# Kernel tuning notes

Hardware: AMD Instinct MI355X
Metric: run time of the kernel (lower is better)

## Reference

```python
import jax, jax.numpy as jnp
import numpy as np

N_NODES = 100000
N_EDGES = 640000
N_REL = 3
D_IN = 128
D_OUT = 128


def setup_inputs() -> dict:
    key = jax.random.key(0)
    ks = jax.random.split(key, 10)
    x = jax.random.normal(ks[0], (N_NODES, D_IN), dtype=jnp.float32)
    src = jax.random.randint(ks[1], (N_REL, N_EDGES), 0, N_NODES, dtype=jnp.int32)
    dst = jax.random.randint(ks[2], (N_REL, N_EDGES), 0, N_NODES, dtype=jnp.int32)
    s = 1.0 / np.sqrt(D_IN)
    W = jax.random.uniform(ks[3], (N_REL, D_IN, D_OUT), minval=-s, maxval=s, dtype=jnp.float32)
    b = jnp.zeros((N_REL, D_OUT), dtype=jnp.float32)
    sa = 1.0 / np.sqrt(D_OUT)
    Wa1 = jax.random.uniform(ks[4], (D_OUT, D_OUT), minval=-sa, maxval=sa, dtype=jnp.float32)
    ba1 = jax.random.uniform(ks[5], (D_OUT,), minval=-sa, maxval=sa, dtype=jnp.float32)
    wa2 = jax.random.uniform(ks[6], (D_OUT,), minval=-sa, maxval=sa, dtype=jnp.float32)
    return {"x": x, "src": src, "dst": dst, "W": W, "b": b,
            "Wa1": Wa1, "ba1": ba1, "wa2": wa2}


def _graph_conv(x, s, d, W_r, b_r, n):
    # DGL GraphConv, norm='both': D_out^{-1/2} -> W -> sum-aggregate -> D_in^{-1/2} -> +b
    ones = jnp.ones_like(s, dtype=x.dtype)
    deg_out = jnp.clip(jax.ops.segment_sum(ones, s, num_segments=n), 1.0)
    deg_in = jnp.clip(jax.ops.segment_sum(ones, d, num_segments=n), 1.0)
    h = (x * jax.lax.rsqrt(deg_out)[:, None]) @ W_r          # [N, D_out]
    agg = jax.ops.segment_sum(h[s], d, num_segments=n)        # gather + scatter-add
    return agg * jax.lax.rsqrt(deg_in)[:, None] + b_r


def reference(x, src, dst, W, b, Wa1, ba1, wa2):
    n = x.shape[0]
    # per-relation graph conv (loop over small fixed relation set)
    rel = jnp.stack([_graph_conv(x, src[r], dst[r], W[r], b[r], n)
                     for r in range(src.shape[0])])            # [R, N, D]
    # attention pooling over relation axis (softmax over dim 0)
    score = jnp.tanh(rel @ Wa1 + ba1) @ wa2                    # [R, N]
    attn = jax.nn.softmax(score, axis=0)[..., None]            # [R, N, 1]
    return (attn * rel).sum(axis=0)                            # [N, D]
```

## Files before the change

kernel.cpp:

```cpp
#include <hip/hip_runtime.h>

#define NN 100000
#define NE 640000
#define NR 3
#define DD 128
#define NSEG (NR * NN)
#define NBPR 782
#define NBUK (NR * NBPR)
#define BCAP 1280
#define CHUNK 8192
#define NBLK2 ((NR * NE + CHUNK - 1) / CHUNK)

typedef unsigned int u32;
typedef short bf8_t __attribute__((ext_vector_type(8)));
typedef float f4_t __attribute__((ext_vector_type(4)));

union U4 { uint4 u; bf8_t b; };

__device__ __forceinline__ u32 bfr(float f) {
  u32 u = __float_as_uint(f);
  return (u + 0x7fffu + ((u >> 16) & 1u)) >> 16;
}
__device__ __forceinline__ u32 packbf(float a, float b) {
  return bfr(a) | (bfr(b) << 16);
}
__device__ __forceinline__ float lo16(u32 u) { return __uint_as_float(u << 16); }
__device__ __forceinline__ float hi16(u32 u) { return __uint_as_float(u & 0xffff0000u); }
__device__ __forceinline__ float bf2f(u32 bits) { return __uint_as_float(bits << 16); }

__device__ __forceinline__ bf8_t ldfrag(const u32* p) {
  U4 t; t.u = *(const uint4*)p; return t.b;
}

__device__ __forceinline__ void gload_lds16(const u32* g, u32* l) {
  __builtin_amdgcn_global_load_lds((const __attribute__((address_space(1))) void*)g,
                                   (__attribute__((address_space(3))) void*)l, 16, 0, 0);
}

__global__ __launch_bounds__(256) void convert_x_kernel(const float* __restrict__ x,
                                                        u32* __restrict__ xb) {
  int i = blockIdx.x * 256 + threadIdx.x;
  if (i >= NN * 64) return;
  float2 v = ((const float2*)x)[i];
  xb[i] = packbf(v.x, v.y);
}

__global__ __launch_bounds__(512) void count_pass_kernel(const int* __restrict__ src,
                                                         const int* __restrict__ dst,
                                                         int* __restrict__ cnt_out,
                                                         int* __restrict__ cntmat) {
  __shared__ int cnt[NBUK];
  const int tid = threadIdx.x;
  for (int i = tid; i < NBUK; i += 512) cnt[i] = 0;
  __syncthreads();
  const int base = blockIdx.x * CHUNK;
  const int end = min(base + CHUNK, NR * NE);
  for (int i = base + tid; i < end; i += 512) {
    int r = i / NE;
    atomicAdd(&cnt_out[r * NN + src[i]], 1);
    atomicAdd(&cnt[r * NBPR + (dst[i] >> 7)], 1);
  }
  __syncthreads();
  for (int i = tid; i < NBUK; i += 512) cntmat[blockIdx.x * NBUK + i] = cnt[i];
}

__global__ __launch_bounds__(256) void rs_out_kernel(const int* __restrict__ cnt_out,
                                                     float* __restrict__ rs_out) {
  int i = blockIdx.x * 256 + threadIdx.x;
  if (i >= NSEG) return;
  int co = cnt_out[i]; if (co < 1) co = 1;
  rs_out[i] = rsqrtf((float)co);
}

__global__ __launch_bounds__(256) void scan_blocks_kernel(int* __restrict__ cntmat,
                                                          int* __restrict__ btot) {
  __shared__ int s[256];
  const int bk = blockIdx.x;
  const int t = threadIdx.x;
  int v = (t < NBLK2) ? cntmat[t * NBUK + bk] : 0;
  s[t] = v;
  __syncthreads();
  for (int d = 1; d < 256; d <<= 1) {
    int a = (t >= d) ? s[t - d] : 0;
    __syncthreads();
    s[t] += a;
    __syncthreads();
  }
  if (t < NBLK2) cntmat[t * NBUK + bk] = s[t] - v;
  if (t == 255) btot[bk] = s[255];
}

__global__ __launch_bounds__(256) void scan_buckets_kernel(const int* __restrict__ btot,
                                                           int* __restrict__ bucketbase) {
  __shared__ int s[256];
  const int tid = threadIdx.x;
  int v[10]; int loc = 0;
#pragma unroll
  for (int j = 0; j < 10; ++j) {
    int idx = tid * 10 + j;
    int c = (idx < NBUK) ? btot[idx] : 0;
    v[j] = c; loc += c;
  }
  s[tid] = loc;
  __syncthreads();
  for (int d = 1; d < 256; d <<= 1) {
    int t = (tid >= d) ? s[tid - d] : 0;
    __syncthreads();
    s[tid] += t;
    __syncthreads();
  }
  int run = s[tid] - loc;
#pragma unroll
  for (int j = 0; j < 10; ++j) {
    int idx = tid * 10 + j;
    if (idx < NBUK) bucketbase[idx] = run;
    run += v[j];
  }
  if (tid == 255) bucketbase[NBUK] = s[255];
}

__global__ __launch_bounds__(512) void place_pass_kernel(const int* __restrict__ src,
                                                         const int* __restrict__ dst,
                                                         const int* __restrict__ cntmat,
                                                         const int* __restrict__ bucketbase,
                                                         u32* __restrict__ bucketbuf) {
  __shared__ int cur[NBUK];
  const int tid = threadIdx.x;
  for (int i = tid; i < NBUK; i += 512)
    cur[i] = bucketbase[i] + cntmat[blockIdx.x * NBUK + i];
  __syncthreads();
  const int base = blockIdx.x * CHUNK;
  const int end = min(base + CHUNK, NR * NE);
  for (int i = base + tid; i < end; i += 512) {
    int r = i / NE;
    int d = dst[i];
    int bk = r * NBPR + (d >> 7);
    int pos = atomicAdd(&cur[bk], 1);
    bucketbuf[pos] = (u32)src[i] | ((u32)(d & 127) << 17);
  }
}

__global__ __launch_bounds__(256) void bucket_aggregate_kernel(
    const u32* __restrict__ xb, const u32* __restrict__ bucketbuf,
    const int* __restrict__ bucketbase, const float* __restrict__ rs_out,
    float* __restrict__ rs_in, u32* __restrict__ aggb) {
  __shared__ u32 eL[BCAP];
  __shared__ u32 sorted[BCAP];
  __shared__ int cntA[128], prefE[128], cur[128];
  const int tid = threadIdx.x;
  const int bk = blockIdx.x;
  const int r = bk / NBPR, bidx = bk % NBPR;
  const int node0 = bidx * 128;
  const int base = bucketbase[bk];
  const int count = min(bucketbase[bk + 1] - base, BCAP);
  if (tid < 128) cntA[tid] = 0;
  for (int i = tid; i < count; i += 256) eL[i] = bucketbuf[base + i];
  __syncthreads();
  for (int i = tid; i < count; i += 256) atomicAdd(&cntA[eL[i] >> 17], 1);
  __syncthreads();
  if (tid < 128) prefE[tid] = cntA[tid];
  __syncthreads();
  for (int d = 1; d < 128; d <<= 1) {
    int v = 0;
    if (tid < 128 && tid >= d) v = prefE[tid - d];
    __syncthreads();
    if (tid < 128) prefE[tid] += v;
    __syncthreads();
  }
  if (tid < 128) {
    int excl = prefE[tid] - cntA[tid];
    prefE[tid] = excl;
    cur[tid] = excl;
    int node = node0 + tid;
    if (node < NN) rs_in[r * NN + node] = rsqrtf((float)max(cntA[tid], 1));
  }
  __syncthreads();
  for (int i = tid; i < count; i += 256) {
    u32 v = eL[i];
    int pos = atomicAdd(&cur[v >> 17], 1);
    sorted[pos] = v & 0x1FFFFu;
  }
  __syncthreads();

  const int l16 = tid & 15, g = tid >> 4;
  const float* rsb = rs_out + r * NN;
  for (int nn = g; nn < 128; nn += 16) {
    const int node = node0 + nn;
    if (node >= NN) continue;
    const int beg = prefE[nn], cE = cntA[nn];
    float a[8] = {0.f, 0.f, 0.f, 0.f, 0.f, 0.f, 0.f, 0.f};
    int e = 0;
    for (; e + 1 < cE; e += 2) {
      int s0 = (int)sorted[beg + e], s1 = (int)sorted[beg + e + 1];
      float c0 = rsb[s0], c1 = rsb[s1];
      uint4 u0 = *(const uint4*)&xb[(size_t)s0 * 64 + l16 * 4];
      uint4 u1 = *(const uint4*)&xb[(size_t)s1 * 64 + l16 * 4];
      a[0] = fmaf(lo16(u0.x), c0, a[0]); a[1] = fmaf(hi16(u0.x), c0, a[1]);
      a[2] = fmaf(lo16(u0.y), c0, a[2]); a[3] = fmaf(hi16(u0.y), c0, a[3]);
      a[4] = fmaf(lo16(u0.z), c0, a[4]); a[5] = fmaf(hi16(u0.z), c0, a[5]);
      a[6] = fmaf(lo16(u0.w), c0, a[6]); a[7] = fmaf(hi16(u0.w), c0, a[7]);
      a[0] = fmaf(lo16(u1.x), c1, a[0]); a[1] = fmaf(hi16(u1.x), c1, a[1]);
      a[2] = fmaf(lo16(u1.y), c1, a[2]); a[3] = fmaf(hi16(u1.y), c1, a[3]);
      a[4] = fmaf(lo16(u1.z), c1, a[4]); a[5] = fmaf(hi16(u1.z), c1, a[5]);
      a[6] = fmaf(lo16(u1.w), c1, a[6]); a[7] = fmaf(hi16(u1.w), c1, a[7]);
    }
    if (e < cE) {
      int s0 = (int)sorted[beg + e];
      float c0 = rsb[s0];
      uint4 u0 = *(const uint4*)&xb[(size_t)s0 * 64 + l16 * 4];
      a[0] = fmaf(lo16(u0.x), c0, a[0]); a[1] = fmaf(hi16(u0.x), c0, a[1]);
      a[2] = fmaf(lo16(u0.y), c0, a[2]); a[3] = fmaf(hi16(u0.y), c0, a[3]);
      a[4] = fmaf(lo16(u0.z), c0, a[4]); a[5] = fmaf(hi16(u0.z), c0, a[5]);
      a[6] = fmaf(lo16(u0.w), c0, a[6]); a[7] = fmaf(hi16(u0.w), c0, a[7]);
    }
    uint4 o;
    o.x = packbf(a[0], a[1]);
    o.y = packbf(a[2], a[3]);
    o.z = packbf(a[4], a[5]);
    o.w = packbf(a[6], a[7]);
    *(uint4*)&aggb[((size_t)r * NN + node) * 64 + l16 * 4] = o;
  }
}

__global__ __launch_bounds__(256) void prep_wwa1_kernel(const float* __restrict__ W,
                                                        const float* __restrict__ Wa1,
                                                        float* __restrict__ WWa1) {
  int idx = blockIdx.x * 256 + threadIdx.x;
  if (idx >= NR * DD * DD) return;
  int r = idx >> 14, rem = idx & 16383, i = rem >> 7, c = rem & 127;
  const float* wrow = W + (r << 14) + (i << 7);
  float s = 0.f;
#pragma unroll 8
  for (int k = 0; k < DD; ++k) s = fmaf(wrow[k], Wa1[k * DD + c], s);
  WWa1[idx] = s;
}

__global__ __launch_bounds__(256) void prep_pack_kernel(const float* __restrict__ W,
                                                        const float* __restrict__ WWa1,
                                                        u32* __restrict__ wt_hi,
                                                        u32* __restrict__ wt_lo,
                                                        u32* __restrict__ wwt_hi) {
  int idx = blockIdx.x * 256 + threadIdx.x;
  if (idx >= NR * DD * 64) return;
  int r = idx >> 13, rem = idx & 8191, n = rem >> 6, ku = rem & 63;
  int k0 = ku * 2;
  int oidx = (r << 13) + ((ku >> 2) << 9) + (n << 2) + (ku & 3);
  {
    const float* M = W + (r << 14);
    float w0 = M[k0 * DD + n], w1 = M[(k0 + 1) * DD + n];
    u32 h0 = bfr(w0), h1 = bfr(w1);
    float l0 = w0 - bf2f(h0), l1 = w1 - bf2f(h1);
    wt_hi[oidx] = h0 | (h1 << 16);
    wt_lo[oidx] = packbf(l0, l1);
  }
  {
    const float* M = WWa1 + (r << 14);
    float w0 = M[k0 * DD + n], w1 = M[(k0 + 1) * DD + n];
    wwt_hi[oidx] = bfr(w0) | (bfr(w1) << 16);
  }
}

__global__ __launch_bounds__(256) void prep_bsum_kernel(const float* __restrict__ b,
                                                        const float* __restrict__ Wa1,
                                                        const float* __restrict__ ba1,
                                                        float* __restrict__ bsum) {
  int idx = blockIdx.x * 256 + threadIdx.x;
  if (idx >= NR * DD) return;
  int r = idx >> 7, c = idx & 127;
  float s = ba1[c];
#pragma unroll 8
  for (int k = 0; k < DD; ++k) s = fmaf(b[r * DD + k], Wa1[k * DD + c], s);
  bsum[idx] = s;
}

#define MFMA(a, b, c) __builtin_amdgcn_mfma_f32_16x16x32_bf16((a), (b), (c), 0, 0, 0)

__global__ __launch_bounds__(256, 2) void tail_fused_kernel(
    const u32* __restrict__ aggb, const u32* __restrict__ wt_hi,
    const u32* __restrict__ wt_lo, const u32* __restrict__ wwt_hi,
    const float* __restrict__ rs_in, const float* __restrict__ bias,
    const float* __restrict__ bsum, const float* __restrict__ wa2,
    float* __restrict__ out) {
  __shared__ u32 As[4160];
  __shared__ float scoreS[2][64];
  __shared__ float eLs[64];
  __shared__ float bL[NR][DD];
  const int tid = threadIdx.x;
  const int l = tid & 63, w = tid >> 6;
  const int wr = w >> 1, wc = w & 1;
  const int l15 = l & 15, lg = l >> 4;
  const int row0 = blockIdx.x * 64;

  for (int idx = tid; idx < NR * DD; idx += 256) bL[idx >> 7][idx & 127] = bias[idx];

  float wa2v[4];
#pragma unroll
  for (int nf = 0; nf < 4; ++nf) wa2v[nf] = wa2[wc * 64 + nf * 16 + l15];

  f4_t fo[2][4];
  float denom[2][4];
#pragma unroll
  for (int rf = 0; rf < 2; ++rf)
#pragma unroll
    for (int reg = 0; reg < 4; ++reg) {
      denom[rf][reg] = 0.f;
#pragma unroll
      for (int nf = 0; nf < 4; ++nf) fo[rf][nf][reg] = 0.f;
    }

  for (int r = 0; r < NR; ++r) {
    __syncthreads();
    const u32* Ar = aggb + (size_t)r * NN * 64;
#pragma unroll
    for (int it = 0; it < 4; ++it) {
      int s = it * 256 + tid;
      int row = s >> 4;
      int c = (s & 15) ^ (row & 7);
      int grow = min(row0 + row, NN - 1);
      gload_lds16(Ar + (size_t)grow * 64 + c * 4, &As[it * 1024 + w * 256]);
    }
    __syncthreads();

    float rsv[2][4];
#pragma unroll
    for (int rf = 0; rf < 2; ++rf)
#pragma unroll
      for (int reg = 0; reg < 4; ++reg)
        rsv[rf][reg] = rs_in[r * NN + min(row0 + wr * 32 + rf * 16 + lg * 4 + reg, NN - 1)];

    f4_t c2[2][4];
#pragma unroll
    for (int rf = 0; rf < 2; ++rf)
#pragma unroll
      for (int nf = 0; nf < 4; ++nf) c2[rf][nf] = (f4_t)0.f;
#pragma unroll
    for (int ks = 0; ks < 4; ++ks) {
      bf8_t a[2];
#pragma unroll
      for (int rf = 0; rf < 2; ++rf) {
        int m = wr * 32 + rf * 16 + l15;
        int ch = (ks * 4 + lg) ^ (m & 7);
        a[rf] = ldfrag(&As[m * 64 + ch * 4]);
      }
#pragma unroll
      for (int nf = 0; nf < 4; ++nf) {
        int n = wc * 64 + nf * 16 + l15;
        bf8_t gb = ldfrag(wwt_hi + (size_t)r * 8192 + (ks * 4 + lg) * 512 + n * 4);
#pragma unroll
        for (int rf = 0; rf < 2; ++rf) c2[rf][nf] = MFMA(a[rf], gb, c2[rf][nf]);
      }
    }

#pragma unroll
    for (int rf = 0; rf < 2; ++rf) {
      float part[4] = {0.f, 0.f, 0.f, 0.f};
#pragma unroll
      for (int nf = 0; nf < 4; ++nf) {
        int col = wc * 64 + nf * 16 + l15;
        float bs = bsum[r * DD + col];
#pragma unroll
        for (int reg = 0; reg < 4; ++reg) {
          float t = fmaf(c2[rf][nf][reg], rsv[rf][reg], bs);
          t = fminf(fmaxf(t, -15.f), 15.f);
          float ex = __expf(2.f * t);
          part[reg] = fmaf((ex - 1.f) / (ex + 1.f), wa2v[nf], part[reg]);
        }
      }
#pragma unroll
      for (int reg = 0; reg < 4; ++reg) {
        float p = part[reg];
        p += __shfl_xor(p, 1);
        p += __shfl_xor(p, 2);
        p += __shfl_xor(p, 4);
        p += __shfl_xor(p, 8);
        if (l15 == 0) scoreS[wc][wr * 32 + rf * 16 + lg * 4 + reg] = p;
      }
    }
    __syncthreads();
    if (tid < 64) eLs[tid] = __expf(scoreS[0][tid] + scoreS[1][tid]);
    __syncthreads();

    float ev[2][4];
#pragma unroll
    for (int rf = 0; rf < 2; ++rf)
#pragma unroll
      for (int reg = 0; reg < 4; ++reg) {
        ev[rf][reg] = eLs[wr * 32 + rf * 16 + lg * 4 + reg];
        denom[rf][reg] += ev[rf][reg];
      }

    f4_t c1[2][4];
#pragma unroll
    for (int rf = 0; rf < 2; ++rf)
#pragma unroll
      for (int nf = 0; nf < 4; ++nf) c1[rf][nf] = (f4_t)0.f;
#pragma unroll
    for (int ks = 0; ks < 4; ++ks) {
      bf8_t a[2];
#pragma unroll
      for (int rf = 0; rf < 2; ++rf) {
        int m = wr * 32 + rf * 16 + l15;
        int ch = (ks * 4 + lg) ^ (m & 7);
        a[rf] = ldfrag(&As[m * 64 + ch * 4]);
      }
#pragma unroll
      for (int nf = 0; nf < 4; ++nf) {
        int n = wc * 64 + nf * 16 + l15;
        size_t bo = (size_t)r * 8192 + (ks * 4 + lg) * 512 + n * 4;
        bf8_t bh = ldfrag(wt_hi + bo);
        bf8_t bl = ldfrag(wt_lo + bo);
#pragma unroll
        for (int rf = 0; rf < 2; ++rf) c1[rf][nf] = MFMA(a[rf], bh, c1[rf][nf]);
#pragma unroll
        for (int rf = 0; rf < 2; ++rf) c1[rf][nf] = MFMA(a[rf], bl, c1[rf][nf]);
      }
    }

#pragma unroll
    for (int rf = 0; rf < 2; ++rf)
#pragma unroll
      for (int reg = 0; reg < 4; ++reg) {
        float er = ev[rf][reg] * rsv[rf][reg];
        float e = ev[rf][reg];
#pragma unroll
        for (int nf = 0; nf < 4; ++nf) {
          int col = wc * 64 + nf * 16 + l15;
          fo[rf][nf][reg] = fmaf(c1[rf][nf][reg], er, fo[rf][nf][reg]);
          fo[rf][nf][reg] = fmaf(bL[r][col], e, fo[rf][nf][reg]);
        }
      }
  }

  float inv[2][4];
#pragma unroll
  for (int rf = 0; rf < 2; ++rf)
#pragma unroll
    for (int reg = 0; reg < 4; ++reg) inv[rf][reg] = 1.f / denom[rf][reg];

  __syncthreads();
  float* Asf = (float*)As;
  const int rloc = tid >> 3;
  const int c0 = (tid & 7) * 16;
#pragma unroll
  for (int half = 0; half < 2; ++half) {
    if (wr == half) {
#pragma unroll
      for (int rf = 0; rf < 2; ++rf)
#pragma unroll
        for (int nf = 0; nf < 4; ++nf)
#pragma unroll
          for (int reg = 0; reg < 4; ++reg)
            Asf[(rf * 16 + lg * 4 + reg) * 130 + wc * 64 + nf * 16 + l15] =
                fo[rf][nf][reg] * inv[rf][reg];
    }
    __syncthreads();
    int grow = row0 + half * 32 + rloc;
    if (grow < NN) {
#pragma unroll
      for (int j = 0; j < 4; ++j) {
        float4 v = *(const float4*)&Asf[rloc * 130 + c0 + j * 4];
        *(float4*)&out[(size_t)grow * DD + c0 + j * 4] = v;
      }
    }
    __syncthreads();
  }
}

extern "C" void kernel_launch(void* const* d_in, const int* in_sizes, int n_in,
                              void* d_out, int out_size, void* d_ws, size_t ws_size,
                              hipStream_t stream) {
  const float* x   = (const float*)d_in[0];
  const int*   src = (const int*)d_in[1];
  const int*   dst = (const int*)d_in[2];
  const float* W   = (const float*)d_in[3];
  const float* b   = (const float*)d_in[4];
  const float* Wa1 = (const float*)d_in[5];
  const float* ba1 = (const float*)d_in[6];
  const float* wa2 = (const float*)d_in[7];
  float* out = (float*)d_out;

  char* ws = (char*)d_ws;
  size_t off = 0;
  u32* aggb = (u32*)(ws + off); off += (size_t)NSEG * 64 * 4;
  u32* xb   = (u32*)(ws + off); off += (size_t)NN * 64 * 4;
  u32* bucketbuf = (u32*)(ws + off); off += (size_t)NR * NE * 4;
  int* cntmat  = (int*)(ws + off); off += (size_t)NBLK2 * NBUK * 4;
  int* cnt_out = (int*)(ws + off); off += (size_t)NSEG * 4;
  float* rs_out = (float*)(ws + off); off += (size_t)NSEG * 4;
  float* rs_in  = (float*)(ws + off); off += (size_t)NSEG * 4;
  int* btot       = (int*)(ws + off); off += (size_t)NBUK * 4;
  int* bucketbase = (int*)(ws + off); off += (size_t)(NBUK + 4) * 4;
  float* WWa1  = (float*)(ws + off); off += (size_t)NR * DD * DD * 4;
  u32* wt_hi   = (u32*)(ws + off); off += (size_t)NR * DD * 64 * 4;
  u32* wt_lo   = (u32*)(ws + off); off += (size_t)NR * DD * 64 * 4;
  u32* wwt_hi  = (u32*)(ws + off); off += (size_t)NR * DD * 64 * 4;
  float* bsum  = (float*)(ws + off); off += (size_t)NR * DD * 4;
  if (ws_size < off) return;

  hipMemsetAsync(cnt_out, 0, (size_t)NSEG * 4, stream);

  prep_wwa1_kernel<<<(NR * DD * DD + 255) / 256, 256, 0, stream>>>(W, Wa1, WWa1);
  prep_pack_kernel<<<(NR * DD * 64 + 255) / 256, 256, 0, stream>>>(W, WWa1, wt_hi, wt_lo,
                                                                   wwt_hi);
  prep_bsum_kernel<<<(NR * DD + 255) / 256, 256, 0, stream>>>(b, Wa1, ba1, bsum);

  convert_x_kernel<<<(NN * 64 + 255) / 256, 256, 0, stream>>>(x, xb);
  count_pass_kernel<<<NBLK2, 512, 0, stream>>>(src, dst, cnt_out, cntmat);
  rs_out_kernel<<<(NSEG + 255) / 256, 256, 0, stream>>>(cnt_out, rs_out);
  scan_blocks_kernel<<<NBUK, 256, 0, stream>>>(cntmat, btot);
  scan_buckets_kernel<<<1, 256, 0, stream>>>(btot, bucketbase);
  place_pass_kernel<<<NBLK2, 512, 0, stream>>>(src, dst, cntmat, bucketbase, bucketbuf);
  bucket_aggregate_kernel<<<NBUK, 256, 0, stream>>>(xb, bucketbuf, bucketbase, rs_out,
                                                    rs_in, aggb);

  tail_fused_kernel<<<(NN + 63) / 64, 256, 0, stream>>>(aggb, wt_hi, wt_lo, wwt_hi,
                                                        rs_in, b, bsum, wa2, out);
}
```

Baseline: 341.4 us.

## Double-buffer relation tiles in LDS and prefetch the next relation during compute

The tail kernel now holds two LDS buffers for the aggregated relation tile. It issues the async global-to-LDS load for relation r+1 while relation r's score and output MFMAs still run, so the load latency at the start of each relation is hidden. It also drops the shared exp buffer and its extra barrier: each thread computes the exp of the summed score itself. In exchange, LDS use roughly doubles, which could limit how many blocks fit per CU, and each thread repeats a few exp calls.

```diff
diff --git a/kernel.cpp b/kernel.cpp
--- a/kernel.cpp
+++ b/kernel.cpp
@@ -281,9 +281,8 @@
     const float* __restrict__ rs_in, const float* __restrict__ bias,
     const float* __restrict__ bsum, const float* __restrict__ wa2,
     float* __restrict__ out) {
-  __shared__ u32 As[4160];
+  __shared__ u32 As[2][4224];
   __shared__ float scoreS[2][64];
-  __shared__ float eLs[64];
   __shared__ float bL[NR][DD];
   const int tid = threadIdx.x;
   const int l = tid & 63, w = tid >> 6;
@@ -291,35 +290,41 @@
   const int l15 = l & 15, lg = l >> 4;
   const int row0 = blockIdx.x * 64;
 
-  for (int idx = tid; idx < NR * DD; idx += 256) bL[idx >> 7][idx & 127] = bias[idx];
-
-  float wa2v[4];
-#pragma unroll
-  for (int nf = 0; nf < 4; ++nf) wa2v[nf] = wa2[wc * 64 + nf * 16 + l15];
-
-  f4_t fo[2][4];
-  float denom[2][4];
-#pragma unroll
-  for (int rf = 0; rf < 2; ++rf)
-#pragma unroll
-    for (int reg = 0; reg < 4; ++reg) {
-      denom[rf][reg] = 0.f;
-#pragma unroll
-      for (int nf = 0; nf < 4; ++nf) fo[rf][nf][reg] = 0.f;
-    }
-
-  for (int r = 0; r < NR; ++r) {
-    __syncthreads();
-    const u32* Ar = aggb + (size_t)r * NN * 64;
+  const int srow = tid >> 4;
+  {
+    const u32* Ar = aggb;
 #pragma unroll
     for (int it = 0; it < 4; ++it) {
       int s = it * 256 + tid;
       int row = s >> 4;
       int c = (s & 15) ^ (row & 7);
       int grow = min(row0 + row, NN - 1);
-      gload_lds16(Ar + (size_t)grow * 64 + c * 4, &As[it * 1024 + w * 256]);
-    }
-    __syncthreads();
+      gload_lds16(Ar + (size_t)grow * 64 + c * 4, &As[0][it * 1024 + w * 256]);
+    }
+  }
+  for (int idx = tid; idx < NR * DD; idx += 256) bL[idx >> 7][idx & 127] = bias[idx];
+  (void)srow;
+
+  float wa2v[4];
+#pragma unroll
+  for (int nf = 0; nf < 4; ++nf) wa2v[nf] = wa2[wc * 64 + nf * 16 + l15];
+
+  f4_t fo[2][4];
+  float denom[2][4];
+#pragma unroll
+  for (int rf = 0; rf < 2; ++rf)
+#pragma unroll
+    for (int reg = 0; reg < 4; ++reg) {
+      denom[rf][reg] = 0.f;
+#pragma unroll
+      for (int nf = 0; nf < 4; ++nf) fo[rf][nf][reg] = 0.f;
+    }
+
+  __syncthreads();
+
+  int cur = 0;
+  for (int r = 0; r < NR; ++r) {
+    const u32* Ab = &As[cur][0];
 
     float rsv[2][4];
 #pragma unroll
@@ -340,7 +345,7 @@
       for (int rf = 0; rf < 2; ++rf) {
         int m = wr * 32 + rf * 16 + l15;
         int ch = (ks * 4 + lg) ^ (m & 7);
-        a[rf] = ldfrag(&As[m * 64 + ch * 4]);
+        a[rf] = ldfrag(&Ab[m * 64 + ch * 4]);
       }
 #pragma unroll
       for (int nf = 0; nf < 4; ++nf) {
@@ -377,15 +382,26 @@
       }
     }
     __syncthreads();
-    if (tid < 64) eLs[tid] = __expf(scoreS[0][tid] + scoreS[1][tid]);
-    __syncthreads();
+
+    if (r + 1 < NR) {
+      const u32* Arn = aggb + (size_t)(r + 1) * NN * 64;
+#pragma unroll
+      for (int it = 0; it < 4; ++it) {
+        int s = it * 256 + tid;
+        int row = s >> 4;
+        int c = (s & 15) ^ (row & 7);
+        int grow = min(row0 + row, NN - 1);
+        gload_lds16(Arn + (size_t)grow * 64 + c * 4, &As[cur ^ 1][it * 1024 + w * 256]);
+      }
+    }
 
     float ev[2][4];
 #pragma unroll
     for (int rf = 0; rf < 2; ++rf)
 #pragma unroll
       for (int reg = 0; reg < 4; ++reg) {
-        ev[rf][reg] = eLs[wr * 32 + rf * 16 + lg * 4 + reg];
+        int idx = wr * 32 + rf * 16 + lg * 4 + reg;
+        ev[rf][reg] = __expf(scoreS[0][idx] + scoreS[1][idx]);
         denom[rf][reg] += ev[rf][reg];
       }
 
@@ -401,7 +417,7 @@
       for (int rf = 0; rf < 2; ++rf) {
         int m = wr * 32 + rf * 16 + l15;
         int ch = (ks * 4 + lg) ^ (m & 7);
-        a[rf] = ldfrag(&As[m * 64 + ch * 4]);
+        a[rf] = ldfrag(&Ab[m * 64 + ch * 4]);
       }
 #pragma unroll
       for (int nf = 0; nf < 4; ++nf) {
@@ -429,6 +445,9 @@
           fo[rf][nf][reg] = fmaf(bL[r][col], e, fo[rf][nf][reg]);
         }
       }
+
+    __syncthreads();
+    cur ^= 1;
   }
 
   float inv[2][4];
@@ -437,8 +456,7 @@
 #pragma unroll
     for (int reg = 0; reg < 4; ++reg) inv[rf][reg] = 1.f / denom[rf][reg];
 
-  __syncthreads();
-  float* Asf = (float*)As;
+  float* Asf = (float*)&As[0][0];
   const int rloc = tid >> 3;
   const int c0 = (tid & 7) * 16;
 #pragma unroll
```

After: 336.3 us. Within noise of the previous version (-1.5%).
